# Performance work log

Hardware: AMD Instinct MI355X
Metric: run time of the kernel (lower is better)

## Reference

```python
import jax, jax.numpy as jnp
from jax import lax
import numpy as np

K = 4            # prototypes per class: 3 kmeans centroids + 1 backbone
EPS = 0.1        # sinkhorn entropic regularization
MAX_ITER = 100
THRESH = 0.01
KM_ITERS = 10    # Lloyd iterations (replaces host-side sklearn KMeans)
HW = 28          # the original reshapes pred to 28x28, fixing n = 784


def setup_inputs():
    key = jax.random.key(0)
    k1, k2, k3, k4 = jax.random.split(key, 4)
    b, n, d, c = 32, HW * HW, 1024, 20
    return {
        "query": jax.random.normal(k1, (b, n, d), dtype=jnp.float32),
        "score": jax.random.uniform(k2, (b, n, c), dtype=jnp.float32),
        "label": jax.random.randint(k3, (b, c), 0, 2),
        "gt": jax.random.randint(k4, (b, HW, HW), 0, c + 1),
        "weights": jnp.array([1.0, 1.0, 0.0, -1.0], dtype=jnp.float32),
    }


def _assign(dq, cen, selfm):
    # dq [b,m,d], cen [b,c,j,d], selfm [b,c,m] float mask -> one-hot labels, counts
    x2 = jnp.sum(dq * dq, axis=-1)                                   # [b,m]
    d2 = (x2[:, None, :, None]
          - 2.0 * jnp.einsum('bmd,bcjd->bcmj', dq, cen)
          + jnp.sum(cen * cen, axis=-1)[:, :, None, :])              # [b,c,m,j]
    oh = jax.nn.one_hot(jnp.argmin(d2, axis=-1), cen.shape[2], dtype=dq.dtype) * selfm[..., None]
    return oh, oh.sum(axis=2)


def _sinkhorn(Km, u, v):
    # vectorized over the [b,c] pair grid, per-pair early exit as in the torch loop
    def cond(st):
        it, r, cc, done = st
        return (it < MAX_ITER) & jnp.logical_not(jnp.all(done))

    def body(st):
        it, r, cc, done = st
        r1 = u / jnp.einsum('bcnj,bcj->bcn', Km, cc)
        c1 = v / jnp.einsum('bcnj,bcn->bcj', Km, r1)
        err = jnp.mean(jnp.abs(r1 - r), axis=-1)                     # [b,c]
        r = jnp.where(done[..., None], r, r1)
        cc = jnp.where(done[..., None], cc, c1)
        done = done | (err < THRESH)
        return it + 1, r, cc, done

    st = (jnp.int32(0), jnp.ones_like(u), jnp.ones_like(v),
          jnp.zeros(Km.shape[:2], dtype=bool))
    _, r, cc, _ = lax.while_loop(cond, body, st)
    return r[..., :, None] * cc[..., None, :] * Km                   # [b,c,n,K]


def _forward(query, score, label, gt, weights):
    b, n, d = query.shape
    c = score.shape[2]
    dq, ds = query[:, ::2, :], score[:, ::2, :]                      # stride-2 downsample
    m = dq.shape[1]
    cls_assign = jnp.argmax(ds, axis=-1)                             # [b,m]
    sel = cls_assign[:, None, :] == jnp.arange(c)[None, :, None]     # [b,c,m]
    selfm = sel.astype(query.dtype)
    cnt = selfm.sum(-1)                                              # [b,c]
    valid = (label > 0) & (cnt >= K)

    # ---- masked Lloyd's k-means with k-1 = 3 clusters per (image, class) pair
    order = jnp.argsort((~sel).astype(jnp.int32), axis=-1)           # masked points first
    init_idx = order[..., :K - 1]                                    # [b,c,3]
    cen = dq[jnp.arange(b)[:, None, None], init_idx]                 # [b,c,3,d]

    def km_step(cen, _):
        oh, kcnt = _assign(dq, cen, selfm)
        sums = jnp.einsum('bmd,bcmj->bcjd', dq, oh)
        cen = jnp.where(kcnt[..., None] > 0,
                        sums / jnp.maximum(kcnt, 1.0)[..., None], cen)
        return cen, None

    cen, _ = lax.scan(km_step, cen, None, length=KM_ITERS)
    oh, kcnt = _assign(dq, cen, selfm)                               # final labels

    # ---- sort centroids by mean cluster score (descending)
    sm = ds.mean(axis=-1)                                            # [b,m]
    avg = jnp.where(kcnt > 0,
                    jnp.einsum('bm,bcmj->bcj', sm, oh) / jnp.maximum(kcnt, 1.0),
                    -jnp.inf)
    ordj = jnp.argsort(-avg, axis=-1)                                # [b,c,3]
    cen = jnp.take_along_axis(cen, ordj[..., None], axis=2)

    # ---- backbone prototype = mean over unselected downsampled tokens
    un = 1.0 - selfm
    backbone = jnp.einsum('bmd,bcm->bcd', dq, un) / jnp.maximum(m - cnt, 1.0)[..., None]
    protos = jnp.concatenate([cen, backbone[:, :, None, :]], axis=2)  # [b,c,4,d]

    # ---- OT between query[0] tokens and the 4 prototypes (original uses query[0] always)
    q0 = query[0]
    q0h = q0 / jnp.maximum(jnp.linalg.norm(q0, axis=-1, keepdims=True), 1e-12)
    ph = protos / jnp.maximum(jnp.linalg.norm(protos, axis=-1, keepdims=True), 1e-12)
    sim = jnp.einsum('nd,bcjd->bcnj', q0h, ph)                       # [b,c,n,4]
    Km = lax.stop_gradient(jnp.exp(-(1.0 - sim) / EPS))              # torch.no_grad
    u = jnp.full((b, c, n), 1.0 / n, dtype=query.dtype)
    v = jnp.full((b, c, K), 1.0 / K, dtype=query.dtype)
    T = lax.stop_gradient(_sinkhorn(Km, u, v))                       # [b,c,n,4]

    valid = valid & jnp.logical_not(jnp.any(jnp.isnan(T), axis=(2, 3)))
    pred = jnp.einsum('bcnj,j->bcn', T, weights)                     # [b,c,n]

    # ---- BCE vs gt masks (28x28 -> 28x28 bilinear resize is the identity)
    y = (gt.reshape(b, -1)[:, None, :] == (jnp.arange(c) + 1)[None, :, None]).astype(pred.dtype)
    p = jnp.clip(pred, 0.0, 1.0)
    bce = -(y * jnp.maximum(jnp.log(p), -100.0)
            + (1.0 - y) * jnp.maximum(jnp.log(1.0 - p), -100.0)).mean(axis=-1)  # [b,c]
    bce = jnp.where(valid, bce, 0.0)
    total_n = valid.sum().astype(pred.dtype)
    return bce.sum() / (total_n + 1e-4)


def reference(query, score, label, gt, weights):
    return _forward(query, score, label, gt, weights)
```

## Files before the change

### kernel.cpp

```cpp
#include <hip/hip_runtime.h>
#include <cmath>

#define BB 32
#define NN 784
#define MM 392
#define DD 1024
#define CC 20
#define JJ 3
#define KP 4
#define KM_ITERS 10
#define GMAX 64
#define SKK 3
#define NCOL (BB * CC * KP)

__global__ void k_cls(const float* __restrict__ score, int* __restrict__ cls,
                      float* __restrict__ sm, int* __restrict__ cnt) {
  int t = blockIdx.x * blockDim.x + threadIdx.x;
  if (t >= BB * MM) return;
  int b = t / MM, i = t - b * MM;
  const float* s = score + ((size_t)b * NN + 2 * i) * CC;
  float best = s[0]; int bi = 0; float acc = s[0];
  #pragma unroll
  for (int c = 1; c < CC; c++) { float v = s[c]; acc += v; if (v > best) { best = v; bi = c; } }
  cls[t] = bi;
  sm[t] = acc / (float)CC;
  atomicAdd(&cnt[b * CC + bi], 1);
}

__global__ void k_valid(const int* __restrict__ label, const int* __restrict__ cnt,
                        int* __restrict__ vlist, int* __restrict__ cpos, int* __restrict__ nvp) {
  __shared__ int sf[1024];
  int t = threadIdx.x;
  int flag = 0;
  if (t < BB * CC) flag = (label[t] > 0 && cnt[t] >= KP) ? 1 : 0;
  sf[t] = flag;
  __syncthreads();
  for (int off = 1; off < 1024; off <<= 1) {
    int v = sf[t];
    int add = (t >= off) ? sf[t - off] : 0;
    __syncthreads();
    sf[t] = v + add;
    __syncthreads();
  }
  if (t < BB * CC) {
    int pos = sf[t] - flag;
    cpos[t] = flag ? pos : -1;
    if (flag) vlist[pos] = t;
  }
  if (t == 0) *nvp = sf[BB * CC - 1];
}

__global__ __launch_bounds__(512) void k_gram(
    const float* __restrict__ query, const int* __restrict__ cls,
    const int* __restrict__ cpos, const float* __restrict__ sm,
    float* __restrict__ classsum, float* __restrict__ ph) {
  int bc = blockIdx.x; int b = bc / CC, c = bc - b * CC;
  int tid = threadIdx.x, lane = tid & 63, wv = tid >> 6;
  const float* qb = query + (size_t)b * NN * DD;
  __shared__ int s_scan[512];
  __shared__ int s_list[GMAX];
  __shared__ __align__(16) float Xs[GMAX][68];
  __shared__ float Gl[GMAX][65];
  __shared__ float s_w[JJ][GMAX];
  __shared__ int s_rank[JJ];

  int flag = 0;
  if (tid < MM) flag = (cls[b * MM + tid] == c) ? 1 : 0;
  s_scan[tid] = flag;
  __syncthreads();
  for (int off = 1; off < 512; off <<= 1) {
    int v = s_scan[tid];
    int add = (tid >= off) ? s_scan[tid - off] : 0;
    __syncthreads();
    s_scan[tid] = v + add;
    __syncthreads();
  }
  if (tid < MM && flag) { int pp = s_scan[tid] - 1; if (pp < GMAX) s_list[pp] = tid; }
  __syncthreads();
  int mc = s_scan[MM - 1]; if (mc > GMAX) mc = GMAX;
  bool valid = (cpos[bc] >= 0);

  const float* pbase0 = nullptr; const float* pbase1 = nullptr;
  float* xdst0 = nullptr; float* xdst1 = nullptr;
  {
    int e0 = tid;
    if (e0 < mc * 16) {
      pbase0 = qb + (size_t)(2 * s_list[e0 >> 4]) * DD + (e0 & 15) * 4;
      xdst0 = &Xs[e0 >> 4][(e0 & 15) * 4];
    }
    int e1 = tid + 512;
    if (e1 < mc * 16) {
      pbase1 = qb + (size_t)(2 * s_list[e1 >> 4]) * DD + (e1 & 15) * 4;
      xdst1 = &Xs[e1 >> 4][(e1 & 15) * 4];
    }
  }

  int npairs = mc * (mc + 1) / 2;
  int pi[5], pj[5];
  float pacc[5];
  #pragma unroll
  for (int s = 0; s < 5; s++) {
    pacc[s] = 0.f; pi[s] = -1; pj[s] = 0;
    int p = tid + s * 512;
    if (valid && p < npairs) {
      int i = (int)floorf((sqrtf(8.0f * (float)p + 1.0f) - 1.0f) * 0.5f);
      while ((i + 1) * (i + 2) / 2 <= p) i++;
      while (i * (i + 1) / 2 > p) i--;
      pi[s] = i; pj[s] = p - i * (i + 1) / 2;
    }
  }

  float4 cur0, cur1, nxt0, nxt1;
  if (pbase0) cur0 = *(const float4*)(pbase0);
  if (pbase1) cur1 = *(const float4*)(pbase1);
  for (int ch = 0; ch < 16; ch++) {
    __syncthreads();
    if (pbase0) *(float4*)xdst0 = cur0;
    if (pbase1) *(float4*)xdst1 = cur1;
    if (ch < 15) {
      if (pbase0) nxt0 = *(const float4*)(pbase0 + (ch + 1) * 64);
      if (pbase1) nxt1 = *(const float4*)(pbase1 + (ch + 1) * 64);
    }
    __syncthreads();
    #pragma unroll
    for (int s = 0; s < 5; s++) {
      if (pi[s] >= 0) {
        const float4* xi = (const float4*)&Xs[pi[s]][0];
        const float4* xj = (const float4*)&Xs[pj[s]][0];
        float a = 0.f;
        #pragma unroll
        for (int kk = 0; kk < 16; kk++) {
          float4 u = xi[kk], w = xj[kk];
          a += u.x * w.x + u.y * w.y + u.z * w.z + u.w * w.w;
        }
        pacc[s] += a;
      }
    }
    if (tid >= 448) {
      int col = tid - 448;
      float ssum = 0.f;
      for (int row = 0; row < mc; row++) ssum += Xs[row][col];
      classsum[(size_t)bc * DD + ch * 64 + col] = ssum;
    }
    cur0 = nxt0; cur1 = nxt1;
  }
  if (!valid) return;

  #pragma unroll
  for (int s = 0; s < 5; s++)
    if (pi[s] >= 0) { Gl[pi[s]][pj[s]] = pacc[s]; Gl[pj[s]][pi[s]] = pacc[s]; }
  __syncthreads();

  if (wv == 0) {
    bool act = lane < mc;
    float smv = act ? sm[b * MM + s_list[lane]] : 0.f;
    s_w[0][lane] = (lane == 0) ? 1.f : 0.f;
    s_w[1][lane] = (lane == 1) ? 1.f : 0.f;
    s_w[2][lane] = (lane == 2) ? 1.f : 0.f;
    int aj = 0, n0 = 0, n1 = 0, n2 = 0;
    for (int it = 0; it <= KM_ITERS; it++) {
      float h0 = 0.f, h1 = 0.f, h2 = 0.f;
      if (act) {
        for (int i = 0; i < mc; i++) {
          float g = Gl[lane][i];
          h0 += s_w[0][i] * g; h1 += s_w[1][i] * g; h2 += s_w[2][i] * g;
        }
      }
      float t0 = s_w[0][lane] * h0, t1 = s_w[1][lane] * h1, t2 = s_w[2][lane] * h2;
      for (int o = 1; o < 64; o <<= 1) {
        t0 += __shfl_xor(t0, o, 64); t1 += __shfl_xor(t1, o, 64); t2 += __shfl_xor(t2, o, 64);
      }
      float e0 = t0 - 2.f * h0, e1 = t1 - 2.f * h1, e2 = t2 - 2.f * h2;
      aj = 0; float bv = e0;
      if (e1 < bv) { bv = e1; aj = 1; }
      if (e2 < bv) { bv = e2; aj = 2; }
      n0 = __popcll(__ballot(act && aj == 0));
      n1 = __popcll(__ballot(act && aj == 1));
      n2 = __popcll(__ballot(act && aj == 2));
      if (it == KM_ITERS) break;
      if (act) {
        if (n0 > 0) s_w[0][lane] = (aj == 0) ? 1.f / (float)n0 : 0.f;
        if (n1 > 0) s_w[1][lane] = (aj == 1) ? 1.f / (float)n1 : 0.f;
        if (n2 > 0) s_w[2][lane] = (aj == 2) ? 1.f / (float)n2 : 0.f;
      }
    }
    float s0 = (act && aj == 0) ? smv : 0.f;
    float s1 = (act && aj == 1) ? smv : 0.f;
    float s2 = (act && aj == 2) ? smv : 0.f;
    for (int o = 1; o < 64; o <<= 1) {
      s0 += __shfl_xor(s0, o, 64); s1 += __shfl_xor(s1, o, 64); s2 += __shfl_xor(s2, o, 64);
    }
    if (lane == 0) {
      float avg[JJ];
      avg[0] = (n0 > 0) ? s0 / (float)n0 : -INFINITY;
      avg[1] = (n1 > 0) ? s1 / (float)n1 : -INFINITY;
      avg[2] = (n2 > 0) ? s2 / (float)n2 : -INFINITY;
      bool used[JJ] = {false, false, false};
      for (int s = 0; s < JJ; s++) {
        int bi = -1; float bv = 0.f;
        for (int j = 0; j < JJ; j++)
          if (!used[j] && (bi < 0 || avg[j] > bv)) { bi = j; bv = avg[j]; }
        used[bi] = true; s_rank[bi] = s;
      }
    }
  }
  __syncthreads();

  float cenv[16];
  if (pbase0) cur0 = *(const float4*)(pbase0);
  if (pbase1) cur1 = *(const float4*)(pbase1);
  for (int ch = 0; ch < 16; ch++) {
    __syncthreads();
    if (pbase0) *(float4*)xdst0 = cur0;
    if (pbase1) *(float4*)xdst1 = cur1;
    if (ch < 15) {
      if (pbase0) nxt0 = *(const float4*)(pbase0 + (ch + 1) * 64);
      if (pbase1) nxt1 = *(const float4*)(pbase1 + (ch + 1) * 64);
    }
    __syncthreads();
    if (tid < 192) {
      int j = tid >> 6, l = tid & 63;
      float a = 0.f;
      for (int g = 0; g < mc; g++) a += s_w[j][g] * Xs[g][l];
      cenv[ch] = a;
    }
    cur0 = nxt0; cur1 = nxt1;
  }
  if (tid < 192) {
    int j = tid >> 6, l = tid & 63;
    float ssq = 0.f;
    #pragma unroll
    for (int ch = 0; ch < 16; ch++) ssq += cenv[ch] * cenv[ch];
    for (int o = 1; o < 64; o <<= 1) ssq += __shfl_xor(ssq, o, 64);
    float nrm = fmaxf(sqrtf(ssq), 1e-12f);
    float* dst = ph + ((size_t)bc * KP + s_rank[j]) * DD + l;
    #pragma unroll
    for (int ch = 0; ch < 16; ch++) dst[ch * 64] = cenv[ch] / nrm;
  }
}

__global__ __launch_bounds__(256) void k_backbone(const float* __restrict__ classsum,
    const int* __restrict__ cpos, const int* __restrict__ cnt, float* __restrict__ ph) {
  int bc = blockIdx.x;
  if (cpos[bc] < 0) return;
  int b = bc / CC;
  int tid = threadIdx.x, lane = tid & 63, wv = tid >> 6;
  __shared__ float s_red[4];
  __shared__ float s_nrm;
  float4 ts = make_float4(0.f, 0.f, 0.f, 0.f);
  for (int c2 = 0; c2 < CC; c2++) {
    float4 v = *(const float4*)(classsum + ((size_t)(b * CC + c2)) * DD + tid * 4);
    ts.x += v.x; ts.y += v.y; ts.z += v.z; ts.w += v.w;
  }
  float4 cs = *(const float4*)(classsum + (size_t)bc * DD + tid * 4);
  float denom = fmaxf((float)(MM - cnt[bc]), 1.f);
  float4 v = make_float4((ts.x - cs.x) / denom, (ts.y - cs.y) / denom,
                         (ts.z - cs.z) / denom, (ts.w - cs.w) / denom);
  float pp = v.x * v.x + v.y * v.y + v.z * v.z + v.w * v.w;
  for (int o = 1; o < 64; o <<= 1) pp += __shfl_xor(pp, o, 64);
  if (lane == 0) s_red[wv] = pp;
  __syncthreads();
  if (tid == 0) s_nrm = fmaxf(sqrtf(s_red[0] + s_red[1] + s_red[2] + s_red[3]), 1e-12f);
  __syncthreads();
  float nrm = s_nrm;
  *(float4*)(ph + ((size_t)bc * KP + 3) * DD + tid * 4) =
      make_float4(v.x / nrm, v.y / nrm, v.z / nrm, v.w / nrm);
}

__global__ void k_q0h(const float* __restrict__ query, float* __restrict__ q0h) {
  int n = blockIdx.x;
  const float* src = query + (size_t)n * DD;
  float ss = 0.f;
  for (int k = threadIdx.x; k < DD; k += 64) { float v = src[k]; ss += v * v; }
  for (int o = 32; o > 0; o >>= 1) ss += __shfl_xor(ss, o, 64);
  float nrm = fmaxf(sqrtf(ss), 1e-12f);
  for (int k = threadIdx.x; k < DD; k += 64) q0h[(size_t)n * DD + k] = src[k] / nrm;
}

__global__ __launch_bounds__(256) void k_gemm(const float* __restrict__ A,
    const float* __restrict__ ph, const int* __restrict__ vlist,
    const int* __restrict__ nvp, float* __restrict__ P) {
  int nv4 = 4 * *nvp;
  int n0 = blockIdx.y * 64;
  if (n0 >= nv4) return;
  __shared__ float As[64][20];
  __shared__ float Bs[64][20];
  int tx = threadIdx.x & 15, ty = threadIdx.x >> 4;
  int m0 = blockIdx.x * 64;
  int s = blockIdx.z;
  int lrow = threadIdx.x >> 2;
  int lk = (threadIdx.x & 3) * 4;
  int brow = n0 + lrow;
  bool bval = brow < nv4;
  const float* Brow = ph;
  if (bval) {
    int bcc = brow >> 2;
    Brow = ph + ((size_t)vlist[bcc] * KP + (brow & 3)) * DD;
  }
  float acc[4][4] = {};
  int kbase = s * 352;
  int kend = (kbase + 352 < DD) ? (kbase + 352) : DD;
  for (int k0 = kbase; k0 < kend; k0 += 16) {
    int ar = m0 + lrow;
    float4 av = (ar < NN) ? *(const float4*)(A + (size_t)ar * DD + k0 + lk)
                          : make_float4(0.f, 0.f, 0.f, 0.f);
    *(float4*)&As[lrow][lk] = av;
    float4 bv = bval ? *(const float4*)(Brow + k0 + lk)
                     : make_float4(0.f, 0.f, 0.f, 0.f);
    *(float4*)&Bs[lrow][lk] = bv;
    __syncthreads();
    #pragma unroll
    for (int kk = 0; kk < 16; kk += 4) {
      float4 a4[4], b4[4];
      #pragma unroll
      for (int i = 0; i < 4; i++) a4[i] = *(const float4*)&As[ty * 4 + i][kk];
      #pragma unroll
      for (int j = 0; j < 4; j++) b4[j] = *(const float4*)&Bs[tx + 16 * j][kk];
      #pragma unroll
      for (int i = 0; i < 4; i++)
        #pragma unroll
        for (int j = 0; j < 4; j++) {
          acc[i][j] += a4[i].x * b4[j].x;
          acc[i][j] += a4[i].y * b4[j].y;
          acc[i][j] += a4[i].z * b4[j].z;
          acc[i][j] += a4[i].w * b4[j].w;
        }
    }
    __syncthreads();
  }
  #pragma unroll
  for (int j = 0; j < 4; j++) {
    int col = n0 + tx + 16 * j;
    float4 o4 = make_float4(acc[0][j], acc[1][j], acc[2][j], acc[3][j]);
    *(float4*)(P + ((size_t)s * NCOL + col) * NN + m0 + ty * 4) = o4;
  }
}

__global__ __launch_bounds__(256) void k_sink(const float* __restrict__ P,
    const int* __restrict__ cpos, const int* __restrict__ gt,
    const float* __restrict__ wts, float* __restrict__ bce, int* __restrict__ vld) {
  int bc = blockIdx.x; int b = bc / CC, c = bc - b * CC;
  int tid = threadIdx.x;
  if (cpos[bc] < 0) {
    if (tid == 0) { bce[bc] = 0.f; vld[bc] = 0; }
    return;
  }
  int p = cpos[bc];
  int lane = tid & 63, wv = tid >> 6;
  __shared__ float ccv[KP];
  __shared__ float wred[4][5];
  __shared__ float s_err;
  __shared__ int s_nan;
  float4 kv[4]; float rr[4];
  #pragma unroll
  for (int s4 = 0; s4 < 4; s4++) {
    int n = tid + 256 * s4;
    kv[s4] = make_float4(0.f, 0.f, 0.f, 0.f); rr[s4] = 1.f;
    if (n < NN) {
      float v[KP] = {0.f, 0.f, 0.f, 0.f};
      #pragma unroll
      for (int s = 0; s < SKK; s++)
        #pragma unroll
        for (int q = 0; q < KP; q++)
          v[q] += P[((size_t)s * NCOL + 4 * p + q) * NN + n];
      float4 o;
      o.x = expf(-(1.0f - v[0]) / 0.1f);
      o.y = expf(-(1.0f - v[1]) / 0.1f);
      o.z = expf(-(1.0f - v[2]) / 0.1f);
      o.w = expf(-(1.0f - v[3]) / 0.1f);
      kv[s4] = o;
    }
  }
  if (tid < KP) ccv[tid] = 1.f;
  if (tid == 0) s_nan = 0;
  __syncthreads();
  const float uu = 1.0f / (float)NN, vv = 1.0f / (float)KP;
  for (int it = 0; it < 100; it++) {
    float c0 = ccv[0], c1 = ccv[1], c2 = ccv[2], c3 = ccv[3];
    float dsum = 0.f, p0 = 0.f, p1 = 0.f, p2 = 0.f, p3 = 0.f;
    #pragma unroll
    for (int s4 = 0; s4 < 4; s4++) {
      int n = tid + 256 * s4;
      if (n < NN) {
        float4 k4 = kv[s4];
        float S = k4.x * c0 + k4.y * c1 + k4.z * c2 + k4.w * c3;
        float r1 = uu / S;
        dsum += fabsf(r1 - rr[s4]);
        rr[s4] = r1;
        p0 += k4.x * r1; p1 += k4.y * r1; p2 += k4.z * r1; p3 += k4.w * r1;
      }
    }
    for (int o = 32; o > 0; o >>= 1) {
      dsum += __shfl_down(dsum, o, 64);
      p0 += __shfl_down(p0, o, 64); p1 += __shfl_down(p1, o, 64);
      p2 += __shfl_down(p2, o, 64); p3 += __shfl_down(p3, o, 64);
    }
    if (lane == 0) { wred[wv][0] = dsum; wred[wv][1] = p0; wred[wv][2] = p1; wred[wv][3] = p2; wred[wv][4] = p3; }
    __syncthreads();
    if (tid == 0) {
      float d = 0.f, q0 = 0.f, q1 = 0.f, q2 = 0.f, q3 = 0.f;
      for (int w = 0; w < 4; w++) { d += wred[w][0]; q0 += wred[w][1]; q1 += wred[w][2]; q2 += wred[w][3]; q3 += wred[w][4]; }
      ccv[0] = vv / q0; ccv[1] = vv / q1; ccv[2] = vv / q2; ccv[3] = vv / q3;
      s_err = d / (float)NN;
    }
    __syncthreads();
    if (s_err < 0.01f) break;
  }
  float w0 = wts[0], w1 = wts[1], w2 = wts[2], w3 = wts[3];
  float cc0 = ccv[0], cc1 = ccv[1], cc2 = ccv[2], cc3 = ccv[3];
  float bsum = 0.f; int nanloc = 0;
  const int* gtb = gt + b * NN;
  #pragma unroll
  for (int s4 = 0; s4 < 4; s4++) {
    int n = tid + 256 * s4;
    if (n < NN) {
      float4 k4 = kv[s4];
      float rv = rr[s4];
      float T0 = rv * cc0 * k4.x, T1 = rv * cc1 * k4.y, T2 = rv * cc2 * k4.z, T3 = rv * cc3 * k4.w;
      if (T0 != T0 || T1 != T1 || T2 != T2 || T3 != T3) nanloc = 1;
      float pred = T0 * w0 + T1 * w1 + T2 * w2 + T3 * w3;
      float pcl = fminf(fmaxf(pred, 0.f), 1.f);
      float t = (gtb[n] == c + 1) ? fmaxf(logf(pcl), -100.f) : fmaxf(logf(1.f - pcl), -100.f);
      bsum += t;
    }
  }
  if (nanloc) s_nan = 1;
  for (int o = 32; o > 0; o >>= 1) bsum += __shfl_down(bsum, o, 64);
  if (lane == 0) wred[wv][0] = bsum;
  __syncthreads();
  if (tid == 0) {
    float tot = wred[0][0] + wred[1][0] + wred[2][0] + wred[3][0];
    if (s_nan) { bce[bc] = 0.f; vld[bc] = 0; }
    else { bce[bc] = -(tot / (float)NN); vld[bc] = 1; }
  }
}

__global__ void k_final(const float* __restrict__ bce, const int* __restrict__ vld,
                        float* __restrict__ out) {
  __shared__ float rs[256];
  __shared__ float rc[256];
  float s = 0.f, cv = 0.f;
  for (int t = threadIdx.x; t < BB * CC; t += 256) { s += bce[t]; cv += (float)vld[t]; }
  rs[threadIdx.x] = s; rc[threadIdx.x] = cv; __syncthreads();
  for (int o = 128; o > 0; o >>= 1) {
    if (threadIdx.x < o) { rs[threadIdx.x] += rs[threadIdx.x + o]; rc[threadIdx.x] += rc[threadIdx.x + o]; }
    __syncthreads();
  }
  if (threadIdx.x == 0) out[0] = rs[0] / (rc[0] + 0.0001f);
}

extern "C" void kernel_launch(void* const* d_in, const int* in_sizes, int n_in,
                              void* d_out, int out_size, void* d_ws, size_t ws_size,
                              hipStream_t stream) {
  (void)in_sizes; (void)n_in; (void)out_size; (void)ws_size;
  const float* query = (const float*)d_in[0];
  const float* score = (const float*)d_in[1];
  const int*   label = (const int*)d_in[2];
  const int*   gt    = (const int*)d_in[3];
  const float* wts   = (const float*)d_in[4];
  float* ws = (float*)d_ws;

  size_t off = 0;
  int* cls = (int*)(ws + off);       off += (size_t)BB * MM;
  int* cnt = (int*)(ws + off);       off += (size_t)BB * CC;
  float* sm = ws + off;              off += (size_t)BB * MM;
  int* vlist = (int*)(ws + off);     off += (size_t)BB * CC;
  int* cpos = (int*)(ws + off);      off += (size_t)BB * CC;
  int* nvp = (int*)(ws + off);       off += 16;
  float* classsum = ws + off;        off += (size_t)BB * CC * DD;
  float* ph = ws + off;              off += (size_t)BB * CC * KP * DD;
  float* q0h = ws + off;             off += (size_t)NN * DD;
  float* P = ws + off;               off += (size_t)SKK * NN * NCOL;
  float* bce = ws + off;             off += (size_t)BB * CC;
  int* vld = (int*)(ws + off);       off += (size_t)BB * CC;

  hipMemsetAsync(cnt, 0, (size_t)BB * CC * sizeof(int), stream);
  k_cls<<<(BB * MM + 255) / 256, 256, 0, stream>>>(score, cls, sm, cnt);
  k_valid<<<1, 1024, 0, stream>>>(label, cnt, vlist, cpos, nvp);
  k_gram<<<BB * CC, 512, 0, stream>>>(query, cls, cpos, sm, classsum, ph);
  k_backbone<<<BB * CC, 256, 0, stream>>>(classsum, cpos, cnt, ph);
  k_q0h<<<NN, 64, 0, stream>>>(query, q0h);
  dim3 gg((NN + 63) / 64, (BB * CC * KP) / 64, SKK);
  k_gemm<<<gg, 256, 0, stream>>>(q0h, ph, vlist, nvp, P);
  k_sink<<<BB * CC, 256, 0, stream>>>(P, cpos, gt, wts, bce, vld);
  k_final<<<1, 256, 0, stream>>>(bce, vld, (float*)d_out);
}
```

Before: 281.5 us.

## Split class sums into own kernel, register-tile Gram, early-exit invalid classes

Moves the per-class column sums out of k_gram into a new k_csum kernel that streams every even query row once per batch and scatters into shared per-class accumulators. This lets k_gram return immediately for invalid classes. k_gram now replaces its block-wide prefix scan with a ballot/popcount compaction, uses 128-wide chunks, and computes the Gram matrix in 2x2 register tiles for more data reuse. Centroids are built by reading query rows directly from global memory, skipping zero weights, instead of re-staging all rows through shared memory. The cost is an extra kernel launch, more shared memory per block, and uncoalesced gather reads in the centroid step.

```diff
diff --git a/kernel.cpp b/kernel.cpp
--- a/kernel.cpp
+++ b/kernel.cpp
@@ -50,105 +50,139 @@
   if (t == 0) *nvp = sf[BB * CC - 1];
 }
 
+__global__ __launch_bounds__(256) void k_csum(const float* __restrict__ query,
+    const int* __restrict__ cls, float* __restrict__ classsum) {
+  int b = blockIdx.x, ch = blockIdx.y;
+  int tid = threadIdx.x, lane = tid & 63, wv = tid >> 6;
+  __shared__ float acc[4][CC][64];
+  __shared__ int s_cls[MM];
+  #pragma unroll
+  for (int c = 0; c < CC; c++) acc[wv][c][lane] = 0.f;
+  for (int i = tid; i < MM; i += 256) s_cls[i] = cls[b * MM + i];
+  __syncthreads();
+  const float* qb = query + (size_t)b * NN * DD + ch * 64 + lane;
+  int i0 = wv * 98;
+  #pragma unroll 4
+  for (int r = 0; r < 98; r++) {
+    int i = i0 + r;
+    float v = qb[(size_t)(2 * i) * DD];
+    int cl = s_cls[i];
+    acc[wv][cl][lane] += v;
+  }
+  __syncthreads();
+  for (int cc = wv; cc < CC; cc += 4) {
+    float s = acc[0][cc][lane] + acc[1][cc][lane] + acc[2][cc][lane] + acc[3][cc][lane];
+    classsum[((size_t)(b * CC + cc)) * DD + ch * 64 + lane] = s;
+  }
+}
+
 __global__ __launch_bounds__(512) void k_gram(
     const float* __restrict__ query, const int* __restrict__ cls,
     const int* __restrict__ cpos, const float* __restrict__ sm,
-    float* __restrict__ classsum, float* __restrict__ ph) {
-  int bc = blockIdx.x; int b = bc / CC, c = bc - b * CC;
+    float* __restrict__ ph) {
+  int bc = blockIdx.x;
+  if (cpos[bc] < 0) return;
+  int b = bc / CC, c = bc - b * CC;
   int tid = threadIdx.x, lane = tid & 63, wv = tid >> 6;
   const float* qb = query + (size_t)b * NN * DD;
-  __shared__ int s_scan[512];
+  __shared__ int s_wtot[8];
   __shared__ int s_list[GMAX];
-  __shared__ __align__(16) float Xs[GMAX][68];
+  __shared__ __align__(16) float Xs[GMAX][132];
   __shared__ float Gl[GMAX][65];
   __shared__ float s_w[JJ][GMAX];
   __shared__ int s_rank[JJ];
+  __shared__ float s_red2[6];
 
   int flag = 0;
   if (tid < MM) flag = (cls[b * MM + tid] == c) ? 1 : 0;
-  s_scan[tid] = flag;
-  __syncthreads();
-  for (int off = 1; off < 512; off <<= 1) {
-    int v = s_scan[tid];
-    int add = (tid >= off) ? s_scan[tid - off] : 0;
-    __syncthreads();
-    s_scan[tid] = v + add;
-    __syncthreads();
-  }
-  if (tid < MM && flag) { int pp = s_scan[tid] - 1; if (pp < GMAX) s_list[pp] = tid; }
-  __syncthreads();
-  int mc = s_scan[MM - 1]; if (mc > GMAX) mc = GMAX;
-  bool valid = (cpos[bc] >= 0);
-
-  const float* pbase0 = nullptr; const float* pbase1 = nullptr;
-  float* xdst0 = nullptr; float* xdst1 = nullptr;
-  {
-    int e0 = tid;
-    if (e0 < mc * 16) {
-      pbase0 = qb + (size_t)(2 * s_list[e0 >> 4]) * DD + (e0 & 15) * 4;
-      xdst0 = &Xs[e0 >> 4][(e0 & 15) * 4];
-    }
-    int e1 = tid + 512;
-    if (e1 < mc * 16) {
-      pbase1 = qb + (size_t)(2 * s_list[e1 >> 4]) * DD + (e1 & 15) * 4;
-      xdst1 = &Xs[e1 >> 4][(e1 & 15) * 4];
-    }
-  }
-
-  int npairs = mc * (mc + 1) / 2;
-  int pi[5], pj[5];
-  float pacc[5];
-  #pragma unroll
-  for (int s = 0; s < 5; s++) {
-    pacc[s] = 0.f; pi[s] = -1; pj[s] = 0;
+  unsigned long long msk = __ballot(flag);
+  int wp = __popcll(msk & ((1ull << lane) - 1ull));
+  if (lane == 0) s_wtot[wv] = __popcll(msk);
+  __syncthreads();
+  int off = 0, mtot = 0;
+  #pragma unroll
+  for (int w = 0; w < 8; w++) { int t = s_wtot[w]; if (w < wv) off += t; mtot += t; }
+  int mc = mtot > GMAX ? GMAX : mtot;
+  if (flag) { int pos = off + wp; if (pos < GMAX) s_list[pos] = tid; }
+  __syncthreads();
+
+  const float* pb[4] = {nullptr, nullptr, nullptr, nullptr};
+  float* xd[4] = {nullptr, nullptr, nullptr, nullptr};
+  #pragma unroll
+  for (int s = 0; s < 4; s++) {
+    int e = tid + s * 512;
+    if (e < mc * 32) {
+      pb[s] = qb + (size_t)(2 * s_list[e >> 5]) * DD + (e & 31) * 4;
+      xd[s] = &Xs[e >> 5][(e & 31) * 4];
+    }
+  }
+
+  int T = (mc + 1) >> 1;
+  int ntile = T * (T + 1) / 2;
+  int ti_[2], tj_[2];
+  float a00[2], a01[2], a10[2], a11[2];
+  #pragma unroll
+  for (int s = 0; s < 2; s++) {
+    ti_[s] = -1; tj_[s] = 0;
+    a00[s] = 0.f; a01[s] = 0.f; a10[s] = 0.f; a11[s] = 0.f;
     int p = tid + s * 512;
-    if (valid && p < npairs) {
+    if (p < ntile) {
       int i = (int)floorf((sqrtf(8.0f * (float)p + 1.0f) - 1.0f) * 0.5f);
       while ((i + 1) * (i + 2) / 2 <= p) i++;
       while (i * (i + 1) / 2 > p) i--;
-      pi[s] = i; pj[s] = p - i * (i + 1) / 2;
-    }
-  }
-
-  float4 cur0, cur1, nxt0, nxt1;
-  if (pbase0) cur0 = *(const float4*)(pbase0);
-  if (pbase1) cur1 = *(const float4*)(pbase1);
-  for (int ch = 0; ch < 16; ch++) {
-    __syncthreads();
-    if (pbase0) *(float4*)xdst0 = cur0;
-    if (pbase1) *(float4*)xdst1 = cur1;
-    if (ch < 15) {
-      if (pbase0) nxt0 = *(const float4*)(pbase0 + (ch + 1) * 64);
-      if (pbase1) nxt1 = *(const float4*)(pbase1 + (ch + 1) * 64);
-    }
+      ti_[s] = i; tj_[s] = p - i * (i + 1) / 2;
+    }
+  }
+
+  float4 cur[4], nxt[4];
+  #pragma unroll
+  for (int s = 0; s < 4; s++) {
+    cur[s] = make_float4(0.f, 0.f, 0.f, 0.f);
+    nxt[s] = make_float4(0.f, 0.f, 0.f, 0.f);
+    if (pb[s]) cur[s] = *(const float4*)(pb[s]);
+  }
+  for (int ch = 0; ch < 8; ch++) {
     __syncthreads();
     #pragma unroll
-    for (int s = 0; s < 5; s++) {
-      if (pi[s] >= 0) {
-        const float4* xi = (const float4*)&Xs[pi[s]][0];
-        const float4* xj = (const float4*)&Xs[pj[s]][0];
-        float a = 0.f;
+    for (int s = 0; s < 4; s++) if (pb[s]) *(float4*)xd[s] = cur[s];
+    if (ch < 7) {
+      #pragma unroll
+      for (int s = 0; s < 4; s++) if (pb[s]) nxt[s] = *(const float4*)(pb[s] + (ch + 1) * 128);
+    }
+    __syncthreads();
+    #pragma unroll
+    for (int s = 0; s < 2; s++) {
+      if (ti_[s] >= 0) {
+        const float4* xr0 = (const float4*)&Xs[2 * ti_[s]][0];
+        const float4* xr1 = (const float4*)&Xs[2 * ti_[s] + 1][0];
+        const float4* xc0 = (const float4*)&Xs[2 * tj_[s]][0];
+        const float4* xc1 = (const float4*)&Xs[2 * tj_[s] + 1][0];
+        float s00 = 0.f, s01 = 0.f, s10 = 0.f, s11 = 0.f;
         #pragma unroll
-        for (int kk = 0; kk < 16; kk++) {
-          float4 u = xi[kk], w = xj[kk];
-          a += u.x * w.x + u.y * w.y + u.z * w.z + u.w * w.w;
+        for (int kk = 0; kk < 32; kk++) {
+          float4 u0 = xr0[kk], u1 = xr1[kk], w0 = xc0[kk], w1 = xc1[kk];
+          s00 += u0.x * w0.x + u0.y * w0.y + u0.z * w0.z + u0.w * w0.w;
+          s01 += u0.x * w1.x + u0.y * w1.y + u0.z * w1.z + u0.w * w1.w;
+          s10 += u1.x * w0.x + u1.y * w0.y + u1.z * w0.z + u1.w * w0.w;
+          s11 += u1.x * w1.x + u1.y * w1.y + u1.z * w1.z + u1.w * w1.w;
         }
-        pacc[s] += a;
-      }
-    }
-    if (tid >= 448) {
-      int col = tid - 448;
-      float ssum = 0.f;
-      for (int row = 0; row < mc; row++) ssum += Xs[row][col];
-      classsum[(size_t)bc * DD + ch * 64 + col] = ssum;
-    }
-    cur0 = nxt0; cur1 = nxt1;
-  }
-  if (!valid) return;
-
-  #pragma unroll
-  for (int s = 0; s < 5; s++)
-    if (pi[s] >= 0) { Gl[pi[s]][pj[s]] = pacc[s]; Gl[pj[s]][pi[s]] = pacc[s]; }
+        a00[s] += s00; a01[s] += s01; a10[s] += s10; a11[s] += s11;
+      }
+    }
+    #pragma unroll
+    for (int s = 0; s < 4; s++) cur[s] = nxt[s];
+  }
+
+  #pragma unroll
+  for (int s = 0; s < 2; s++) {
+    if (ti_[s] >= 0) {
+      int r0 = 2 * ti_[s], r1 = r0 + 1, c0 = 2 * tj_[s], c1 = c0 + 1;
+      if (r0 < mc && c0 < mc) { Gl[r0][c0] = a00[s]; Gl[c0][r0] = a00[s]; }
+      if (r0 < mc && c1 < mc) { Gl[r0][c1] = a01[s]; Gl[c1][r0] = a01[s]; }
+      if (r1 < mc && c0 < mc) { Gl[r1][c0] = a10[s]; Gl[c0][r1] = a10[s]; }
+      if (r1 < mc && c1 < mc) { Gl[r1][c1] = a11[s]; Gl[c1][r1] = a11[s]; }
+    }
+  }
   __syncthreads();
 
   if (wv == 0) {
@@ -206,36 +240,31 @@
   }
   __syncthreads();
 
-  float cenv[16];
-  if (pbase0) cur0 = *(const float4*)(pbase0);
-  if (pbase1) cur1 = *(const float4*)(pbase1);
-  for (int ch = 0; ch < 16; ch++) {
-    __syncthreads();
-    if (pbase0) *(float4*)xdst0 = cur0;
-    if (pbase1) *(float4*)xdst1 = cur1;
-    if (ch < 15) {
-      if (pbase0) nxt0 = *(const float4*)(pbase0 + (ch + 1) * 64);
-      if (pbase1) nxt1 = *(const float4*)(pbase1 + (ch + 1) * 64);
-    }
-    __syncthreads();
-    if (tid < 192) {
-      int j = tid >> 6, l = tid & 63;
-      float a = 0.f;
-      for (int g = 0; g < mc; g++) a += s_w[j][g] * Xs[g][l];
-      cenv[ch] = a;
-    }
-    cur0 = nxt0; cur1 = nxt1;
-  }
-  if (tid < 192) {
-    int j = tid >> 6, l = tid & 63;
-    float ssq = 0.f;
+  float4 a0 = make_float4(0.f, 0.f, 0.f, 0.f), a1 = make_float4(0.f, 0.f, 0.f, 0.f);
+  int j = tid >> 7, q = tid & 127;
+  if (tid < 384) {
+    for (int g = 0; g < mc; g++) {
+      float w = s_w[j][g];
+      if (w != 0.f) {
+        const float4* row = (const float4*)(qb + (size_t)(2 * s_list[g]) * DD);
+        float4 v0 = row[q], v1 = row[q + 128];
+        a0.x += w * v0.x; a0.y += w * v0.y; a0.z += w * v0.z; a0.w += w * v0.w;
+        a1.x += w * v1.x; a1.y += w * v1.y; a1.z += w * v1.z; a1.w += w * v1.w;
+      }
+    }
+    float ssq = a0.x * a0.x + a0.y * a0.y + a0.z * a0.z + a0.w * a0.w
+              + a1.x * a1.x + a1.y * a1.y + a1.z * a1.z + a1.w * a1.w;
     #pragma unroll
-    for (int ch = 0; ch < 16; ch++) ssq += cenv[ch] * cenv[ch];
     for (int o = 1; o < 64; o <<= 1) ssq += __shfl_xor(ssq, o, 64);
-    float nrm = fmaxf(sqrtf(ssq), 1e-12f);
-    float* dst = ph + ((size_t)bc * KP + s_rank[j]) * DD + l;
-    #pragma unroll
-    for (int ch = 0; ch < 16; ch++) dst[ch * 64] = cenv[ch] / nrm;
+    if (lane == 0) s_red2[wv] = ssq;
+  }
+  __syncthreads();
+  if (tid < 384) {
+    float nrm = fmaxf(sqrtf(s_red2[2 * j] + s_red2[2 * j + 1]), 1e-12f);
+    float4* dst = (float4*)(ph + ((size_t)bc * KP + s_rank[j]) * DD);
+    float4 o0 = make_float4(a0.x / nrm, a0.y / nrm, a0.z / nrm, a0.w / nrm);
+    float4 o1 = make_float4(a1.x / nrm, a1.y / nrm, a1.z / nrm, a1.w / nrm);
+    dst[q] = o0; dst[q + 128] = o1;
   }
 }
 
@@ -477,7 +506,8 @@
   hipMemsetAsync(cnt, 0, (size_t)BB * CC * sizeof(int), stream);
   k_cls<<<(BB * MM + 255) / 256, 256, 0, stream>>>(score, cls, sm, cnt);
   k_valid<<<1, 1024, 0, stream>>>(label, cnt, vlist, cpos, nvp);
-  k_gram<<<BB * CC, 512, 0, stream>>>(query, cls, cpos, sm, classsum, ph);
+  k_csum<<<dim3(BB, 16), 256, 0, stream>>>(query, cls, classsum);
+  k_gram<<<BB * CC, 512, 0, stream>>>(query, cls, cpos, sm, ph);
   k_backbone<<<BB * CC, 256, 0, stream>>>(classsum, cpos, cnt, ph);
   k_q0h<<<NN, 64, 0, stream>>>(query, q0h);
   dim3 gg((NN + 63) / 64, (BB * CC * KP) / 64, SKK);
```

After: 301.1 us. 1.07x slower.
